# Kernel tuning notes

Measured on AMD Instinct MI355X. Metric: run time of the kernel, lower is better.

## Reference

```python
import jax, jax.numpy as jnp
import numpy as np

B, S, E, H = 4, 1024, 1024, 16
HD = E // H  # 64


def setup_inputs() -> dict:
    key = jax.random.key(0)
    ks = jax.random.split(key, 9)
    scale = 1.0 / np.sqrt(E)
    x = jax.random.normal(ks[0], (B, S, E), dtype=jnp.float32)
    attention_mask = jnp.ones((B, S, S), dtype=jnp.int32)
    # per-head projection weights, batched over heads: [H, E, HD]
    Wq = jax.random.normal(ks[1], (H, E, HD), dtype=jnp.float32) * scale
    Wk = jax.random.normal(ks[2], (H, E, HD), dtype=jnp.float32) * scale
    Wv = jax.random.normal(ks[3], (H, E, HD), dtype=jnp.float32) * scale
    bq = jax.random.normal(ks[4], (H, HD), dtype=jnp.float32) * scale
    bk = jax.random.normal(ks[5], (H, HD), dtype=jnp.float32) * scale
    bv = jax.random.normal(ks[6], (H, HD), dtype=jnp.float32) * scale
    # output projection, torch Linear convention: [out_features, in_features]
    Wo = jax.random.normal(ks[7], (E, E), dtype=jnp.float32) * scale
    bo = jax.random.normal(ks[8], (E,), dtype=jnp.float32) * scale
    return {"x": x, "attention_mask": attention_mask, "Wq": Wq, "bq": bq,
            "Wk": Wk, "bk": bk, "Wv": Wv, "bv": bv, "Wo": Wo, "bo": bo}


def reference(x, attention_mask, Wq, bq, Wk, bk, Wv, bv, Wo, bo):
    # batched-over-heads QKV projections: (B,S,E) x (H,E,HD) -> (B,H,S,HD)
    q = jnp.einsum('bse,hed->bhsd', x, Wq) + bq[None, :, None, :]
    k = jnp.einsum('bse,hed->bhsd', x, Wk) + bk[None, :, None, :]
    v = jnp.einsum('bse,hed->bhsd', x, Wv) + bv[None, :, None, :]
    scores = jnp.einsum('bhsd,bhtd->bhst', q, k) / jnp.sqrt(jnp.float32(HD))
    mask = attention_mask[:, None, :, :]  # (B,1,S,S) broadcast over heads
    scores = jnp.where(mask == 0, -jnp.inf, scores)
    weights = jax.nn.softmax(scores, axis=-1)
    out = jnp.einsum('bhst,bhtd->bhsd', weights, v)
    # concat heads on last dim: (B,S,H*HD) == (B,S,E)
    out = out.transpose(0, 2, 1, 3).reshape(B, S, E)
    return out @ Wo.T + bo
```

## Files before the change

kernel.cpp:

```cpp
#include <hip/hip_runtime.h>
#include <hip/hip_bf16.h>

#define NB 4
#define SEQ 1024
#define EMB 1024
#define NH 16
#define HD 64

typedef unsigned short u16;
typedef __attribute__((ext_vector_type(8))) __bf16 bf16x8;
typedef __attribute__((ext_vector_type(8))) short short8;
typedef __attribute__((ext_vector_type(4))) float floatx4;

__device__ inline u16 f2b_rn(float f) {
    union { float f; unsigned int i; } x; x.f = f;
    unsigned int r = (x.i + 0x7FFFu + ((x.i >> 16) & 1u)) >> 16;
    return (u16)r;
}
__device__ inline bf16x8 s2b(short8 v) {
    union { short8 s; bf16x8 b; } x; x.s = v; return x.b;
}

__device__ inline void gload_lds16(const void* g, void* l) {
    __builtin_amdgcn_global_load_lds(
        (const __attribute__((address_space(1))) void*)g,
        (__attribute__((address_space(3))) void*)l, 16, 0, 0);
}

__device__ inline bf16x8 ldsfrag(const u16* base, int r, int c) {
    return s2b(*(const short8*)&base[r * 64 + (c ^ ((r & 7) * 8))]);
}

__device__ inline void cvt8(const float* __restrict__ s, u16* __restrict__ d) {
    float4 a = *(const float4*)(s);
    float4 b = *(const float4*)(s + 4);
    union { u16 u[8]; int4 v; } o;
    o.u[0] = f2b_rn(a.x); o.u[1] = f2b_rn(a.y); o.u[2] = f2b_rn(a.z); o.u[3] = f2b_rn(a.w);
    o.u[4] = f2b_rn(b.x); o.u[5] = f2b_rn(b.y); o.u[6] = f2b_rn(b.z); o.u[7] = f2b_rn(b.w);
    *(int4*)(d) = o.v;
}

__global__ __launch_bounds__(256) void prep(
    const float* __restrict__ x, const float* __restrict__ Wq,
    const float* __restrict__ Wk, const float* __restrict__ Wv,
    const float* __restrict__ Wo, const int* __restrict__ mask,
    u16* __restrict__ xb, u16* __restrict__ Wt, u16* __restrict__ Wob,
    unsigned long long* __restrict__ bits)
{
    __shared__ u16 T[64 * 80];
    int bx = blockIdx.x;
    int tid = threadIdx.x;

    if (bx < 2048) {
        int i = bx * 2048 + tid * 8;
        cvt8(x + i, xb + i);
    } else if (bx < 2560) {
        int i = (bx - 2048) * 2048 + tid * 8;
        cvt8(Wo + i, Wob + i);
    } else if (bx < 3328) {
        int bx2 = bx - 2560;
        int e0 = (bx2 & 15) * 64;
        int ph = bx2 >> 4;
        int p = ph >> 4, h = ph & 15;
        const float* W = (p == 0 ? Wq : (p == 1 ? Wk : Wv)) + h * (EMB * HD);
        #pragma unroll
        for (int c = 0; c < 2; ++c) {
            int flat = c * 2048 + tid * 8;
            int r = flat >> 6;
            int d = flat & 63;
            cvt8(W + (size_t)(e0 + r) * HD + d, &T[r * 80 + d]);
        }
        __syncthreads();
        int d = tid >> 2;
        int ec = tid & 3;
        union { u16 u[16]; int4 v[2]; } tmp;
        #pragma unroll
        for (int i = 0; i < 16; ++i) tmp.u[i] = T[(ec * 16 + i) * 80 + d];
        u16* dst = Wt + ((size_t)(p * NH + h) * HD + d) * EMB + e0 + ec * 16;
        *(int4*)(dst) = tmp.v[0];
        *(int4*)(dst + 8) = tmp.v[1];
    } else {
        int base = (bx - 3328) * 64 + (tid >> 6) * 16;
        int lane = tid & 63;
        #pragma unroll
        for (int i = 0; i < 16; ++i) {
            int gw = base + i;
            int m = mask[(size_t)gw * 64 + lane];
            unsigned long long bl = __ballot(m != 0);
            if (lane == 0) bits[gw] = bl;
        }
    }
}

__global__ __launch_bounds__(256) void qkv_gemm(
    const u16* __restrict__ x,
    const u16* __restrict__ Wt2,
    const float* __restrict__ bq, const float* __restrict__ bk, const float* __restrict__ bv,
    u16* __restrict__ Q, u16* __restrict__ K, u16* __restrict__ Vt)
{
    __shared__ u16 As[128 * 64];
    __shared__ u16 Bs[128 * 64];

    int m0 = blockIdx.x * 128;
    int n0 = blockIdx.y * 128;
    int tid = threadIdx.x;
    int w = tid >> 6, lane = tid & 63, quad = lane >> 4, ln = lane & 15;
    int wm = w & 1, wn = w >> 1;

    floatx4 acc[4][4] = {};

    for (int k0 = 0; k0 < EMB; k0 += 64) {
        __syncthreads();
        #pragma unroll
        for (int i = 0; i < 4; ++i) {
            int flat0 = i * 256 + (tid & 192);
            int flat = flat0 + lane;
            int r = flat >> 3;
            int c = ((flat & 7) ^ (r & 7)) * 8;
            gload_lds16(x   + (size_t)(m0 + r) * EMB + k0 + c, As + flat0 * 8);
            gload_lds16(Wt2 + (size_t)(n0 + r) * EMB + k0 + c, Bs + flat0 * 8);
        }
        __syncthreads();

        #pragma unroll
        for (int kk = 0; kk < 2; ++kk) {
            bf16x8 a[4], bf[4];
            #pragma unroll
            for (int mt = 0; mt < 4; ++mt)
                a[mt] = ldsfrag(As, wm * 64 + mt * 16 + ln, kk * 32 + quad * 8);
            #pragma unroll
            for (int nc = 0; nc < 4; ++nc)
                bf[nc] = ldsfrag(Bs, wn * 64 + nc * 16 + ln, kk * 32 + quad * 8);
            #pragma unroll
            for (int mt = 0; mt < 4; ++mt)
                #pragma unroll
                for (int nc = 0; nc < 4; ++nc)
                    acc[mt][nc] = __builtin_amdgcn_mfma_f32_16x16x32_bf16(a[mt], bf[nc], acc[mt][nc], 0, 0, 0);
        }
    }

    int p = n0 >> 10;
    const float* bias = (p == 0 ? bq : (p == 1 ? bk : bv));
    if (p < 2) {
        u16* Out = (p == 0) ? Q : K;
        float qs = (p == 0) ? 0.125f * 1.44269504f : 1.0f;
        #pragma unroll
        for (int nc = 0; nc < 4; ++nc) {
            int n = n0 + wn * 64 + nc * 16 + ln;
            int h = (n >> 6) & 15, d = n & 63;
            float bv_ = bias[n & 1023];
            #pragma unroll
            for (int mt = 0; mt < 4; ++mt) {
                #pragma unroll
                for (int reg = 0; reg < 4; ++reg) {
                    int m = m0 + wm * 64 + mt * 16 + quad * 4 + reg;
                    int b_ = m >> 10, s = m & 1023;
                    Out[((size_t)(b_ * NH + h) * SEQ + s) * HD + d] = f2b_rn((acc[mt][nc][reg] + bv_) * qs);
                }
            }
        }
    } else {
        #pragma unroll
        for (int nc = 0; nc < 4; ++nc) {
            int n = n0 + wn * 64 + nc * 16 + ln;
            int h = (n >> 6) & 15, d = n & 63;
            float bv_ = bias[n & 1023];
            #pragma unroll
            for (int mt = 0; mt < 4; ++mt) {
                int m = m0 + wm * 64 + mt * 16 + quad * 4;
                int b_ = m >> 10, s = m & 1023;
                union { u16 u[4]; uint2 v; } pk;
                #pragma unroll
                for (int reg = 0; reg < 4; ++reg)
                    pk.u[reg] = f2b_rn(acc[mt][nc][reg] + bv_);
                *(uint2*)&Vt[((size_t)(b_ * NH + h) * HD + d) * SEQ + s] = pk.v;
            }
        }
    }
}

__global__ __launch_bounds__(256) void attn(
    const u16* __restrict__ Q, const u16* __restrict__ K, const u16* __restrict__ Vt,
    const unsigned long long* __restrict__ bits,
    u16* __restrict__ Aout)
{
    const int PP = 72;
    __shared__ u16 Ks[64 * 64];
    __shared__ u16 Vs[72 * 64];
    __shared__ u16 Ps[64 * PP];

    int q0 = blockIdx.x * 64;
    int bh = blockIdx.y;
    int b = bh >> 4, h = bh & 15;
    const u16* Qb = Q  + (size_t)bh * SEQ * HD;
    const u16* Kb = K  + (size_t)bh * SEQ * HD;
    const u16* Vb = Vt + (size_t)bh * HD * SEQ;

    int tid = threadIdx.x;
    int w = tid >> 6, lane = tid & 63, quad = lane >> 4, ln = lane & 15;

    if (tid < 16) *(uint2*)&Vs[64 * 64 + tid * 4] = make_uint2(0x3F803F80u, 0x3F803F80u);

    bf16x8 qf[2];
    {
        const u16* qp = Qb + (size_t)(q0 + w * 16 + ln) * HD + quad * 8;
        union { int4 i; bf16x8 b; } c0, c1;
        c0.i = *(const int4*)(qp);
        c1.i = *(const int4*)(qp + 32);
        qf[0] = c0.b; qf[1] = c1.b;
    }
    const unsigned long long* brow = bits + ((size_t)b * SEQ + q0 + w * 16 + ln) * 16;

    floatx4 o[5] = {};

    for (int tt = 0; tt < SEQ / 64; ++tt) {
        int t0 = tt * 64;
        __syncthreads();
        #pragma unroll
        for (int i = 0; i < 2; ++i) {
            int flat0 = i * 256 + (tid & 192);
            int flat = flat0 + lane;
            int r = flat >> 3;
            int c = ((flat & 7) ^ (r & 7)) * 8;
            gload_lds16(Kb + (size_t)(t0 + r) * HD + c, Ks + flat0 * 8);
            gload_lds16(Vb + (size_t)r * SEQ + t0 + c, Vs + flat0 * 8);
        }
        __syncthreads();

        floatx4 sc[4] = {};
        #pragma unroll
        for (int kk = 0; kk < 2; ++kk) {
            #pragma unroll
            for (int tb = 0; tb < 4; ++tb)
                sc[tb] = __builtin_amdgcn_mfma_f32_16x16x32_bf16(
                    ldsfrag(Ks, tb * 16 + ln, kk * 32 + quad * 8), qf[kk], sc[tb], 0, 0, 0);
        }

        {
            unsigned long long bm = brow[tt];
            if (__any(bm != ~0ull)) {
                #pragma unroll
                for (int tb = 0; tb < 4; ++tb)
                    #pragma unroll
                    for (int reg = 0; reg < 4; ++reg)
                        if (!((bm >> (tb * 16 + quad * 4 + reg)) & 1)) sc[tb][reg] = -1e30f;
            }
        }

        {
            int mrow = w * 16 + ln;
            #pragma unroll
            for (int tb = 0; tb < 4; ++tb) {
                union { float f; unsigned int i; } e0_, e1_, e2_, e3_;
                e0_.f = __builtin_amdgcn_exp2f(sc[tb][0]);
                e1_.f = __builtin_amdgcn_exp2f(sc[tb][1]);
                e2_.f = __builtin_amdgcn_exp2f(sc[tb][2]);
                e3_.f = __builtin_amdgcn_exp2f(sc[tb][3]);
                uint2 pk;
                pk.x = ((e0_.i + 0x8000u) >> 16) | ((e1_.i + 0x8000u) & 0xFFFF0000u);
                pk.y = ((e2_.i + 0x8000u) >> 16) | ((e3_.i + 0x8000u) & 0xFFFF0000u);
                *(uint2*)&Ps[mrow * PP + tb * 16 + quad * 4] = pk;
            }
        }

        #pragma unroll
        for (int kk = 0; kk < 2; ++kk) {
            bf16x8 pf = s2b(*(const short8*)&Ps[(w * 16 + ln) * PP + kk * 32 + quad * 8]);
            #pragma unroll
            for (int dt = 0; dt < 5; ++dt)
                o[dt] = __builtin_amdgcn_mfma_f32_16x16x32_bf16(
                    pf, ldsfrag(Vs, dt * 16 + ln, kk * 32 + quad * 8), o[dt], 0, 0, 0);
        }
    }

    #pragma unroll
    for (int reg = 0; reg < 4; ++reg) {
        float l = __shfl(o[4][reg], lane & 48, 64);
        float inv = 1.0f / l;
        int m = q0 + w * 16 + quad * 4 + reg;
        #pragma unroll
        for (int dt = 0; dt < 4; ++dt)
            Aout[((size_t)b * SEQ + m) * EMB + h * HD + dt * 16 + ln] = f2b_rn(o[dt][reg] * inv);
    }
}

__global__ __launch_bounds__(256) void out_proj(
    const u16* __restrict__ A,
    const u16* __restrict__ Wo,
    const float* __restrict__ bo,
    float* __restrict__ Out)
{
    __shared__ u16 As[64 * 64];
    __shared__ u16 Bs[128 * 64];

    int m0 = blockIdx.x * 64;
    int n0 = blockIdx.y * 128;
    int tid = threadIdx.x;
    int w = tid >> 6, lane = tid & 63, quad = lane >> 4, ln = lane & 15;
    int wm = w & 1, wn = w >> 1;

    floatx4 acc[2][4] = {};

    for (int k0 = 0; k0 < EMB; k0 += 64) {
        __syncthreads();
        #pragma unroll
        for (int i = 0; i < 2; ++i) {
            int flat0 = i * 256 + (tid & 192);
            int flat = flat0 + lane;
            int r = flat >> 3;
            int c = ((flat & 7) ^ (r & 7)) * 8;
            gload_lds16(A + (size_t)(m0 + r) * EMB + k0 + c, As + flat0 * 8);
        }
        #pragma unroll
        for (int i = 0; i < 4; ++i) {
            int flat0 = i * 256 + (tid & 192);
            int flat = flat0 + lane;
            int r = flat >> 3;
            int c = ((flat & 7) ^ (r & 7)) * 8;
            gload_lds16(Wo + (size_t)(n0 + r) * EMB + k0 + c, Bs + flat0 * 8);
        }
        __syncthreads();

        #pragma unroll
        for (int kk = 0; kk < 2; ++kk) {
            bf16x8 a[2], bfr[4];
            #pragma unroll
            for (int mt = 0; mt < 2; ++mt)
                a[mt] = ldsfrag(As, wm * 32 + mt * 16 + ln, kk * 32 + quad * 8);
            #pragma unroll
            for (int nc = 0; nc < 4; ++nc)
                bfr[nc] = ldsfrag(Bs, wn * 64 + nc * 16 + ln, kk * 32 + quad * 8);
            #pragma unroll
            for (int mt = 0; mt < 2; ++mt)
                #pragma unroll
                for (int nc = 0; nc < 4; ++nc)
                    acc[mt][nc] = __builtin_amdgcn_mfma_f32_16x16x32_bf16(a[mt], bfr[nc], acc[mt][nc], 0, 0, 0);
        }
    }

    #pragma unroll
    for (int nc = 0; nc < 4; ++nc) {
        int n = n0 + wn * 64 + nc * 16 + ln;
        float bb = bo[n];
        #pragma unroll
        for (int mt = 0; mt < 2; ++mt) {
            #pragma unroll
            for (int reg = 0; reg < 4; ++reg) {
                int m = m0 + wm * 32 + mt * 16 + quad * 4 + reg;
                Out[(size_t)m * EMB + n] = acc[mt][nc][reg] + bb;
            }
        }
    }
}

extern "C" void kernel_launch(void* const* d_in, const int* in_sizes, int n_in,
                              void* d_out, int out_size, void* d_ws, size_t ws_size,
                              hipStream_t stream) {
    const float* x  = (const float*)d_in[0];
    const int*   mk = (const int*)d_in[1];
    const float* Wq = (const float*)d_in[2];
    const float* bq = (const float*)d_in[3];
    const float* Wk = (const float*)d_in[4];
    const float* bk = (const float*)d_in[5];
    const float* Wv = (const float*)d_in[6];
    const float* bv = (const float*)d_in[7];
    const float* Wo = (const float*)d_in[8];
    const float* bo = (const float*)d_in[9];
    float* out = (float*)d_out;

    const size_t MB = 1u << 20;
    char* ws = (char*)d_ws;
    u16* xb  = (u16*)ws;
    u16* Wt  = (u16*)(ws + 8 * MB);
    u16* Wob = (u16*)(ws + 14 * MB);
    unsigned long long* bits = (unsigned long long*)(ws + 16 * MB);
    u16* Qw  = (u16*)(ws + 16 * MB + 512 * 1024);
    u16* Kw  = (u16*)(ws + 24 * MB + 512 * 1024);
    u16* Vtw = (u16*)(ws + 32 * MB + 512 * 1024);
    u16* Ao  = xb;

    prep<<<4352, 256, 0, stream>>>(x, Wq, Wk, Wv, Wo, mk, xb, Wt, Wob, bits);
    qkv_gemm<<<dim3((NB * SEQ) / 128, 3 * EMB / 128), 256, 0, stream>>>(
        xb, Wt, bq, bk, bv, Qw, Kw, Vtw);
    attn<<<dim3(SEQ / 64, NB * NH), 256, 0, stream>>>(Qw, Kw, Vtw, bits, Ao);
    out_proj<<<dim3((NB * SEQ) / 64, EMB / 128), 256, 0, stream>>>(Ao, Wob, bo, out);
}
```

Measured before the change: 214.3 us.

## Split key tiles across waves in attention with per-wave LDS and final reduction

Each wave now processes every one of the block's 64 query rows, but only its own quarter of the key/value tiles, staged in a private LDS region. This removes the block-wide __syncthreads from the inner loop. The partial outputs and row sums from the four waves are combined through LDS at the end. Row sums are accumulated explicitly from the exponentials instead of through an extra ones-column MFMA. In exchange, LDS per block grows substantially and register pressure rises (16 output accumulators plus 16 score tiles per wave), which reduces occupancy. The s_waitcnt(0) after each load also leaves global-to-LDS latency unhidden inside a wave.

```diff
diff --git a/kernel.cpp b/kernel.cpp
--- a/kernel.cpp
+++ b/kernel.cpp
@@ -184,10 +184,7 @@
     const unsigned long long* __restrict__ bits,
     u16* __restrict__ Aout)
 {
-    const int PP = 72;
-    __shared__ u16 Ks[64 * 64];
-    __shared__ u16 Vs[72 * 64];
-    __shared__ u16 Ps[64 * PP];
+    __shared__ u16 lds[4][9344];
 
     int q0 = blockIdx.x * 64;
     int bh = blockIdx.y;
@@ -199,88 +196,135 @@
     int tid = threadIdx.x;
     int w = tid >> 6, lane = tid & 63, quad = lane >> 4, ln = lane & 15;
 
-    if (tid < 16) *(uint2*)&Vs[64 * 64 + tid * 4] = make_uint2(0x3F803F80u, 0x3F803F80u);
-
-    bf16x8 qf[2];
-    {
-        const u16* qp = Qb + (size_t)(q0 + w * 16 + ln) * HD + quad * 8;
+    u16* KsW = &lds[w][0];
+    u16* VsW = &lds[w][4096];
+    u16* PsW = &lds[w][8192];
+
+    bf16x8 qf[4][2];
+    #pragma unroll
+    for (int mc = 0; mc < 4; ++mc) {
+        const u16* qp = Qb + (size_t)(q0 + mc * 16 + ln) * HD + quad * 8;
         union { int4 i; bf16x8 b; } c0, c1;
         c0.i = *(const int4*)(qp);
         c1.i = *(const int4*)(qp + 32);
-        qf[0] = c0.b; qf[1] = c1.b;
-    }
-    const unsigned long long* brow = bits + ((size_t)b * SEQ + q0 + w * 16 + ln) * 16;
-
-    floatx4 o[5] = {};
-
-    for (int tt = 0; tt < SEQ / 64; ++tt) {
+        qf[mc][0] = c0.b; qf[mc][1] = c1.b;
+    }
+
+    floatx4 o[4][4] = {};
+    float l_acc[4] = {0.f, 0.f, 0.f, 0.f};
+
+    for (int ti = 0; ti < 4; ++ti) {
+        int tt = w * 4 + ti;
         int t0 = tt * 64;
-        __syncthreads();
-        #pragma unroll
-        for (int i = 0; i < 2; ++i) {
-            int flat0 = i * 256 + (tid & 192);
-            int flat = flat0 + lane;
+        __builtin_amdgcn_s_waitcnt(0);
+        #pragma unroll
+        for (int i = 0; i < 8; ++i) {
+            int flat = i * 64 + lane;
             int r = flat >> 3;
             int c = ((flat & 7) ^ (r & 7)) * 8;
-            gload_lds16(Kb + (size_t)(t0 + r) * HD + c, Ks + flat0 * 8);
-            gload_lds16(Vb + (size_t)r * SEQ + t0 + c, Vs + flat0 * 8);
-        }
-        __syncthreads();
-
-        floatx4 sc[4] = {};
+            gload_lds16(Kb + (size_t)(t0 + r) * HD + c, KsW + i * 512);
+            gload_lds16(Vb + (size_t)r * SEQ + t0 + c, VsW + i * 512);
+        }
+        __builtin_amdgcn_s_waitcnt(0);
+
+        floatx4 sc[4][4] = {};
         #pragma unroll
         for (int kk = 0; kk < 2; ++kk) {
+            bf16x8 kf[4];
             #pragma unroll
             for (int tb = 0; tb < 4; ++tb)
-                sc[tb] = __builtin_amdgcn_mfma_f32_16x16x32_bf16(
-                    ldsfrag(Ks, tb * 16 + ln, kk * 32 + quad * 8), qf[kk], sc[tb], 0, 0, 0);
-        }
-
-        {
-            unsigned long long bm = brow[tt];
+                kf[tb] = ldsfrag(KsW, tb * 16 + ln, kk * 32 + quad * 8);
+            #pragma unroll
+            for (int tb = 0; tb < 4; ++tb)
+                #pragma unroll
+                for (int mc = 0; mc < 4; ++mc)
+                    sc[tb][mc] = __builtin_amdgcn_mfma_f32_16x16x32_bf16(
+                        kf[tb], qf[mc][kk], sc[tb][mc], 0, 0, 0);
+        }
+
+        #pragma unroll
+        for (int mc = 0; mc < 4; ++mc) {
+            unsigned long long bm = bits[((size_t)b * SEQ + q0 + mc * 16 + ln) * 16 + tt];
             if (__any(bm != ~0ull)) {
                 #pragma unroll
                 for (int tb = 0; tb < 4; ++tb)
                     #pragma unroll
                     for (int reg = 0; reg < 4; ++reg)
-                        if (!((bm >> (tb * 16 + quad * 4 + reg)) & 1)) sc[tb][reg] = -1e30f;
-            }
-        }
-
-        {
-            int mrow = w * 16 + ln;
+                        if (!((bm >> (tb * 16 + quad * 4 + reg)) & 1)) sc[tb][mc][reg] = -1e30f;
+            }
+        }
+
+        bf16x8 vf[2][4];
+        #pragma unroll
+        for (int kk = 0; kk < 2; ++kk)
+            #pragma unroll
+            for (int dt = 0; dt < 4; ++dt)
+                vf[kk][dt] = ldsfrag(VsW, dt * 16 + ln, kk * 32 + quad * 8);
+
+        #pragma unroll
+        for (int mc = 0; mc < 4; ++mc) {
+            float lp = 0.f;
             #pragma unroll
             for (int tb = 0; tb < 4; ++tb) {
                 union { float f; unsigned int i; } e0_, e1_, e2_, e3_;
-                e0_.f = __builtin_amdgcn_exp2f(sc[tb][0]);
-                e1_.f = __builtin_amdgcn_exp2f(sc[tb][1]);
-                e2_.f = __builtin_amdgcn_exp2f(sc[tb][2]);
-                e3_.f = __builtin_amdgcn_exp2f(sc[tb][3]);
+                e0_.f = __builtin_amdgcn_exp2f(sc[tb][mc][0]);
+                e1_.f = __builtin_amdgcn_exp2f(sc[tb][mc][1]);
+                e2_.f = __builtin_amdgcn_exp2f(sc[tb][mc][2]);
+                e3_.f = __builtin_amdgcn_exp2f(sc[tb][mc][3]);
+                lp += (e0_.f + e1_.f) + (e2_.f + e3_.f);
                 uint2 pk;
                 pk.x = ((e0_.i + 0x8000u) >> 16) | ((e1_.i + 0x8000u) & 0xFFFF0000u);
                 pk.y = ((e2_.i + 0x8000u) >> 16) | ((e3_.i + 0x8000u) & 0xFFFF0000u);
-                *(uint2*)&Ps[mrow * PP + tb * 16 + quad * 4] = pk;
-            }
-        }
-
-        #pragma unroll
-        for (int kk = 0; kk < 2; ++kk) {
-            bf16x8 pf = s2b(*(const short8*)&Ps[(w * 16 + ln) * PP + kk * 32 + quad * 8]);
-            #pragma unroll
-            for (int dt = 0; dt < 5; ++dt)
-                o[dt] = __builtin_amdgcn_mfma_f32_16x16x32_bf16(
-                    pf, ldsfrag(Vs, dt * 16 + ln, kk * 32 + quad * 8), o[dt], 0, 0, 0);
-        }
-    }
-
+                *(uint2*)&PsW[ln * 72 + tb * 16 + quad * 4] = pk;
+            }
+            lp += __shfl_xor(lp, 16, 64);
+            lp += __shfl_xor(lp, 32, 64);
+            l_acc[mc] += lp;
+
+            #pragma unroll
+            for (int kk = 0; kk < 2; ++kk) {
+                bf16x8 pf = s2b(*(const short8*)&PsW[ln * 72 + kk * 32 + quad * 8]);
+                #pragma unroll
+                for (int dt = 0; dt < 4; ++dt)
+                    o[mc][dt] = __builtin_amdgcn_mfma_f32_16x16x32_bf16(
+                        pf, vf[kk][dt], o[mc][dt], 0, 0, 0);
+            }
+        }
+    }
+
+    float* dump = (float*)&lds[w][0];
+    #pragma unroll
+    for (int mc = 0; mc < 4; ++mc)
+        #pragma unroll
+        for (int dt = 0; dt < 4; ++dt)
+            *(floatx4*)&dump[((mc * 4 + dt) * 64 + lane) * 4] = o[mc][dt];
+    {
+        floatx4 lv; lv[0] = l_acc[0]; lv[1] = l_acc[1]; lv[2] = l_acc[2]; lv[3] = l_acc[3];
+        *(floatx4*)&dump[(16 * 64 + lane) * 4] = lv;
+    }
+    __syncthreads();
+
+    floatx4 osum[4] = {};
+    floatx4 lsumv = {};
+    #pragma unroll
+    for (int wp = 0; wp < 4; ++wp) {
+        const float* src = (const float*)&lds[wp][0];
+        #pragma unroll
+        for (int dt = 0; dt < 4; ++dt)
+            osum[dt] += *(const floatx4*)&src[((w * 4 + dt) * 64 + lane) * 4];
+        lsumv += *(const floatx4*)&src[(16 * 64 + lane) * 4];
+    }
+    float l_m = lsumv[w];
+
+    float* Lb = (float*)((char*)&lds[w][0] + 17408);
+    if (quad == 0) Lb[ln] = l_m;
     #pragma unroll
     for (int reg = 0; reg < 4; ++reg) {
-        float l = __shfl(o[4][reg], lane & 48, 64);
-        float inv = 1.0f / l;
+        float inv = 1.0f / Lb[quad * 4 + reg];
         int m = q0 + w * 16 + quad * 4 + reg;
         #pragma unroll
         for (int dt = 0; dt < 4; ++dt)
-            Aout[((size_t)b * SEQ + m) * EMB + h * HD + dt * 16 + ln] = f2b_rn(o[dt][reg] * inv);
+            Aout[((size_t)b * SEQ + m) * EMB + h * HD + dt * 16 + ln] = f2b_rn(osum[dt][reg] * inv);
     }
 }
 
```

Result: slower. 230.6 us (+7.6%).
